# Optimization experiments

Measured on AMD Instinct MI355X. Metric: run time of the kernel, lower is better.

## Reference

```python
import jax, jax.numpy as jnp
import numpy as np

B, IN, H = 4096, 1024, 1024


def setup_inputs() -> dict:
    key = jax.random.key(0)
    ks = jax.random.split(key, 12)
    s = float(np.sqrt(6.0 / (IN + H)))  # xavier-uniform-like scale
    u = lambda k, shp: jax.random.uniform(k, shp, jnp.float32, -s, s)
    return {
        "x": jax.random.normal(ks[0], (B, IN), jnp.float32),
        "h_prev": jax.random.normal(ks[1], (B, H), jnp.float32),
        "c_prev": jax.random.normal(ks[2], (B, H), jnp.float32),
        "n_prev": jnp.ones((B, H), jnp.float32),
        "m_prev": jnp.zeros((B, H), jnp.float32),
        "Wi_x": u(ks[3], (H, IN)), "bi": jnp.zeros((H,), jnp.float32), "Wi_h": u(ks[4], (H, H)),
        "Wf_x": u(ks[5], (H, IN)), "bf": jnp.full((H,), 2.0, jnp.float32), "Wf_h": u(ks[6], (H, H)),
        "Wz_x": u(ks[7], (H, IN)), "bz": jnp.zeros((H,), jnp.float32), "Wz_h": u(ks[8], (H, H)),
        "Wo_x": u(ks[9], (H, IN)), "bo": jnp.zeros((H,), jnp.float32), "Wo_h": u(ks[10], (H, H)),
    }


def reference(x, h_prev, c_prev, n_prev, m_prev,
              Wi_x, bi, Wi_h, Wf_x, bf, Wf_h,
              Wz_x, bz, Wz_h, Wo_x, bo, Wo_h):
    # 8 projections (x-side with bias, h-side without), torch Linear: y = x @ W.T + b
    i_tilde = x @ Wi_x.T + bi + h_prev @ Wi_h.T
    f_aff   = x @ Wf_x.T + bf + h_prev @ Wf_h.T
    z_aff   = x @ Wz_x.T + bz + h_prev @ Wz_h.T
    o_aff   = x @ Wo_x.T + bo + h_prev @ Wo_h.T

    # forget_as_exp=False path: sigmoid forget gate, log-domain stabilizer
    log_f = jnp.log(jnp.clip(jax.nn.sigmoid(f_aff), 1e-8, None))
    m_t = jnp.maximum(log_f + m_prev, i_tilde)
    i_prime = jnp.exp(i_tilde - m_t)
    f_prime = jnp.exp(log_f + m_prev - m_t)

    z = jnp.tanh(z_aff)
    c_t = f_prime * c_prev + i_prime * z
    n_t = f_prime * n_prev + i_prime
    h_t = jax.nn.sigmoid(o_aff) * (c_t / jnp.clip(n_t, 1e-6, None))
    return h_t, c_t, n_t, m_t
```

## Files before the change

### kernel.cpp

```cpp
#include <hip/hip_runtime.h>
#include <stdint.h>


#define B_DIM 4096
#define K_DIM 2048

typedef __bf16 bf16x8 __attribute__((ext_vector_type(8)));
typedef float f32x4 __attribute__((ext_vector_type(4)));
typedef unsigned short ushort8 __attribute__((ext_vector_type(8)));

__device__ __forceinline__ unsigned short f2bf(float f) {
  unsigned u = __float_as_uint(f);
  u += 0x7fffu + ((u >> 16) & 1u);
  return (unsigned short)(u >> 16);
}
__device__ __forceinline__ float bf2f(unsigned short u) {
  return __uint_as_float(((unsigned)u) << 16);
}

__device__ __forceinline__ ushort8 load8_as_bf16(const void* base, size_t off, bool isbf) {
  if (isbf) return *(const ushort8*)((const unsigned short*)base + off);
  const float* f = (const float*)base + off;
  float4 v0 = ((const float4*)f)[0];
  float4 v1 = ((const float4*)f)[1];
  ushort8 o;
  o[0] = f2bf(v0.x); o[1] = f2bf(v0.y); o[2] = f2bf(v0.z); o[3] = f2bf(v0.w);
  o[4] = f2bf(v1.x); o[5] = f2bf(v1.y); o[6] = f2bf(v1.z); o[7] = f2bf(v1.w);
  return o;
}

__global__ void pack_all(const void* __restrict__ xv, const void* __restrict__ hv,
                         const void* __restrict__ Wix, const void* __restrict__ Wih,
                         const void* __restrict__ Wfx, const void* __restrict__ Wfh,
                         const void* __restrict__ Wzx, const void* __restrict__ Wzh,
                         const void* __restrict__ Wox, const void* __restrict__ Woh,
                         unsigned short* __restrict__ Apk, unsigned short* __restrict__ Bpk) {
  const int blk = blockIdx.x;
  const int lane = threadIdx.x & 63;
  const bool isA = blk < 4096;
  const unsigned* disc = (const unsigned*)(isA ? xv : Wix);
  int v = 0;
  if (lane < 32) {
    unsigned e = (disc[lane] >> 7) & 0xFFu;
    v = (e > (isA ? 129u : 122u)) ? 1 : 0;
  }
  const bool isbf = (__ballot(v) == 0ull);

  const int k = threadIdx.x * 8;
  if (isA) {
    const int m = blk;
    const void* src = (k < 1024) ? xv : hv;
    size_t off = (size_t)m * 1024 + (k & 1023);
    *(ushort8*)(Apk + (size_t)m * 2048 + k) = load8_as_bf16(src, off, isbf);
  } else {
    const int br = blk - 4096;
    const int g = (br >> 4) & 3;
    const int wrow = ((br >> 6) << 4) | (br & 15);
    const void* W;
    if (k < 1024) W = (g == 0) ? Wix : (g == 1) ? Wfx : (g == 2) ? Wzx : Wox;
    else          W = (g == 0) ? Wih : (g == 1) ? Wfh : (g == 2) ? Wzh : Woh;
    size_t off = (size_t)wrow * 1024 + (k & 1023);
    *(ushort8*)(Bpk + (size_t)br * 2048 + k) = load8_as_bf16(W, off, isbf);
  }
}


__device__ __forceinline__ void gload16(const unsigned short* g, unsigned short* l) {
  __builtin_amdgcn_global_load_lds(
      (__attribute__((address_space(1))) void*)g,
      (__attribute__((address_space(3))) void*)l, 16, 0, 0);
}

#define SCHED0 __builtin_amdgcn_sched_barrier(0)
#define BAR    __builtin_amdgcn_s_barrier()
#define VM4    asm volatile("s_waitcnt vmcnt(4)" ::: "memory")
#define VM0    asm volatile("s_waitcnt vmcnt(0)" ::: "memory")
#define NOWAIT ((void)0)
#define NOSTAGE ((void)0)
#define LGKM0  { asm volatile("s_waitcnt lgkmcnt(0)" ::: "memory"); SCHED0; }

#define STAGE_HALF(buf, ab, hf, kt) {                                          \
    _Pragma("unroll")                                                          \
    for (int r_ = 0; r_ < 2; ++r_) {                                           \
      const unsigned short* g_ = (ab ? sB : sA) +                              \
          (size_t)((r_ * 128 + (hf) * (ab ? 32 : 64)) * 2048 + (kt) * 64);     \
      gload16(g_, &lds[buf][ab][(hf) * 128 + r_ * 64 + w * 8][0]);             \
    } }

#define RD_A(buf, mh)                                                          \
  _Pragma("unroll")                                                            \
  for (int mi = 0; mi < 4; ++mi) {                                             \
    fA[mi][0] = *(const bf16x8*)(&lds[buf][0][0][0] + ((mh)*128 + mi*16)*64 + aBase + csw0); \
    fA[mi][1] = *(const bf16x8*)(&lds[buf][0][0][0] + ((mh)*128 + mi*16)*64 + aBase + csw1); \
  }
#define RD_B(buf, nh, FB)                                                      \
  _Pragma("unroll")                                                            \
  for (int nf = 0; nf < 2; ++nf) {                                             \
    FB[nf][0] = *(const bf16x8*)(&lds[buf][1][0][0] + ((nh)*128 + nf*16)*64 + bBase + csw0); \
    FB[nf][1] = *(const bf16x8*)(&lds[buf][1][0][0] + ((nh)*128 + nf*16)*64 + bBase + csw1); \
  }

#define MFMA_Q(mh, nh, FB) {                                                   \
    __builtin_amdgcn_s_setprio(1);                                             \
    _Pragma("unroll")                                                          \
    for (int mi = 0; mi < 4; ++mi)                                             \
      _Pragma("unroll")                                                        \
      for (int nf = 0; nf < 2; ++nf)                                           \
        _Pragma("unroll")                                                      \
        for (int ks = 0; ks < 2; ++ks)                                         \
          acc[(mh)*4 + mi][(nh)*2 + nf] = __builtin_amdgcn_mfma_f32_16x16x32_bf16( \
              fA[mi][ks], FB[nf][ks], acc[(mh)*4 + mi][(nh)*2 + nf], 0, 0, 0); \
    __builtin_amdgcn_s_setprio(0);                                             \
  }

#define PH(READS, STAGE, MF, WAIT) {                                           \
    READS; STAGE; SCHED0; BAR; LGKM0; MF; WAIT; SCHED0; BAR; SCHED0; }

__global__ __launch_bounds__(512, 2) void gemm_fused(
    const unsigned short* __restrict__ Apk,
    const unsigned short* __restrict__ Bpk,
    const void* __restrict__ bi, const void* __restrict__ bfg,
    const void* __restrict__ bz, const void* __restrict__ bo,
    const void* __restrict__ c_prev, const void* __restrict__ n_prev,
    const void* __restrict__ m_prev,
    float* __restrict__ out)
{
  __shared__ unsigned short lds[2][2][256][64];

  const int tid  = threadIdx.x;
  const int w    = tid >> 6;
  const int lane = tid & 63;
  const int wm   = w >> 2;
  const int wn   = w & 3;
  const int lcol = lane & 15;

  const int bid = blockIdx.x;
  const int swz = (bid & 7) * 32 + (bid >> 3);
  const int bm = swz >> 4;
  const int bn = swz & 15;

  const int l3 = lane >> 3;
  const int cg = (lane & 7) ^ l3;
  const unsigned short* sA = Apk + (size_t)(bm * 256 + w * 8 + l3) * 2048 + cg * 8;
  const unsigned short* sB = Bpk + (size_t)(bn * 256 + (w >> 2) * 64 + (w & 3) * 8 + l3) * 2048 + cg * 8;

  const int csw0 = (((lane >> 4)    ) ^ (lane & 7)) * 8;
  const int csw1 = ((4 + (lane >> 4)) ^ (lane & 7)) * 8;
  const int aBase = (wm * 64 + lcol) * 64;
  const int bBase = (wn * 32 + lcol) * 64;

  f32x4 acc[8][4] = {};
  bf16x8 fA[4][2], fB0[2][2], fB1[2][2];

  STAGE_HALF(0, 0, 0, 0); SCHED0;
  STAGE_HALF(0, 1, 0, 0); SCHED0;
  STAGE_HALF(0, 0, 1, 0); SCHED0;
  STAGE_HALF(0, 1, 1, 0); SCHED0;
  STAGE_HALF(1, 0, 0, 1); SCHED0;
  STAGE_HALF(1, 1, 0, 1); SCHED0;
  VM4; SCHED0; BAR; SCHED0;

  for (int t = 0; t < 30; t += 2) {
    PH({ RD_A(0, 0); RD_B(0, 0, fB0); }, STAGE_HALF(1, 1, 1, t + 1), MFMA_Q(0, 0, fB0), NOWAIT);
    PH({ RD_B(0, 1, fB1); },             STAGE_HALF(1, 0, 1, t + 1), MFMA_Q(0, 1, fB1), NOWAIT);
    PH({ RD_A(0, 1); },                  STAGE_HALF(0, 0, 0, t + 2), MFMA_Q(1, 1, fB1), NOWAIT);
    PH({ },                              STAGE_HALF(0, 1, 0, t + 2), MFMA_Q(1, 0, fB0), VM4);
    PH({ RD_A(1, 0); RD_B(1, 0, fB0); }, STAGE_HALF(0, 1, 1, t + 2), MFMA_Q(0, 0, fB0), NOWAIT);
    PH({ RD_B(1, 1, fB1); },             STAGE_HALF(0, 0, 1, t + 2), MFMA_Q(0, 1, fB1), NOWAIT);
    PH({ RD_A(1, 1); },                  STAGE_HALF(1, 0, 0, t + 3), MFMA_Q(1, 1, fB1), NOWAIT);
    PH({ },                              STAGE_HALF(1, 1, 0, t + 3), MFMA_Q(1, 0, fB0), VM4);
  }
  PH({ RD_A(0, 0); RD_B(0, 0, fB0); }, STAGE_HALF(1, 1, 1, 31), MFMA_Q(0, 0, fB0), NOWAIT);
  PH({ RD_B(0, 1, fB1); },             STAGE_HALF(1, 0, 1, 31), MFMA_Q(0, 1, fB1), NOWAIT);
  PH({ RD_A(0, 1); },                  NOSTAGE,                 MFMA_Q(1, 1, fB1), NOWAIT);
  PH({ },                              NOSTAGE,                 MFMA_Q(1, 0, fB0), VM0);
  PH({ RD_A(1, 0); RD_B(1, 0, fB0); }, NOSTAGE,                 MFMA_Q(0, 0, fB0), NOWAIT);
  PH({ RD_B(1, 1, fB1); },             NOSTAGE,                 MFMA_Q(0, 1, fB1), NOWAIT);
  PH({ RD_A(1, 1); },                  NOSTAGE,                 MFMA_Q(1, 1, fB1), NOWAIT);
  PH({ },                              NOSTAGE,                 MFMA_Q(1, 0, fB0), NOWAIT);

  const bool sbf = (((const unsigned*)n_prev)[0] == 0x3F803F80u);
  const bool bbf = (((const unsigned*)bfg)[0]    == 0x40004000u);
  const int n = (bn * 4 + wn) * 16 + lcol;
  const float bi_n = bbf ? bf2f(((const unsigned short*)bi)[n])  : ((const float*)bi)[n];
  const float bf_n = bbf ? bf2f(((const unsigned short*)bfg)[n]) : ((const float*)bfg)[n];
  const float bz_n = bbf ? bf2f(((const unsigned short*)bz)[n])  : ((const float*)bz)[n];
  const float bo_n = bbf ? bf2f(((const unsigned short*)bo)[n])  : ((const float*)bo)[n];
  const int row0 = bm * 256 + wm * 128 + (lane >> 4) * 4;

  float* out_h = out;
  float* out_c = out + 4194304;
  float* out_n = out + 2 * 4194304;
  float* out_m = out + 3 * 4194304;

#pragma unroll
  for (int mi = 0; mi < 8; ++mi) {
#pragma unroll
    for (int r = 0; r < 4; ++r) {
      const int row = row0 + mi * 16 + r;
      const size_t idx = (size_t)row * 1024 + n;
      float it = acc[mi][0][r] + bi_n;
      float fa = acc[mi][1][r] + bf_n;
      float za = acc[mi][2][r] + bz_n;
      float oa = acc[mi][3][r] + bo_n;
      float cp  = sbf ? bf2f(((const unsigned short*)c_prev)[idx]) : ((const float*)c_prev)[idx];
      float npv = sbf ? bf2f(((const unsigned short*)n_prev)[idx]) : ((const float*)n_prev)[idx];
      float mp  = sbf ? bf2f(((const unsigned short*)m_prev)[idx]) : ((const float*)m_prev)[idx];

      float sf = 1.f / (1.f + __expf(-fa));
      sf = fmaxf(sf, 1e-8f);
      float lf = __logf(sf);
      float mt = fmaxf(lf + mp, it);
      float ip = __expf(it - mt);
      float fp = __expf(lf + mp - mt);
      float zc = fminf(fmaxf(za, -15.f), 15.f);
      float e2 = __expf(2.f * zc);
      float z  = (e2 - 1.f) / (e2 + 1.f);
      float ct = fp * cp + ip * z;
      float nt = fp * npv + ip;
      float so = 1.f / (1.f + __expf(-oa));
      float ht = so * (ct / fmaxf(nt, 1e-6f));

      out_h[idx] = ht;
      out_c[idx] = ct;
      out_n[idx] = nt;
      out_m[idx] = mt;
    }
  }
}

extern "C" void kernel_launch(void* const* d_in, const int* in_sizes, int n_in,
                              void* d_out, int out_size, void* d_ws, size_t ws_size,
                              hipStream_t stream) {
  const void* x      = d_in[0];
  const void* h_prev = d_in[1];
  const void* c_prev = d_in[2];
  const void* n_prev = d_in[3];
  const void* m_prev = d_in[4];
  const void* Wi_x = d_in[5];
  const void* bi   = d_in[6];
  const void* Wi_h = d_in[7];
  const void* Wf_x = d_in[8];
  const void* bf   = d_in[9];
  const void* Wf_h = d_in[10];
  const void* Wz_x = d_in[11];
  const void* bz   = d_in[12];
  const void* Wz_h = d_in[13];
  const void* Wo_x = d_in[14];
  const void* bo   = d_in[15];
  const void* Wo_h = d_in[16];

  unsigned short* Apk = (unsigned short*)d_ws;
  unsigned short* Bpk = Apk + (size_t)B_DIM * K_DIM;

  pack_all<<<8192, 256, 0, stream>>>(x, h_prev, Wi_x, Wi_h, Wf_x, Wf_h,
                                     Wz_x, Wz_h, Wo_x, Wo_h, Apk, Bpk);
  gemm_fused<<<256, 512, 0, stream>>>(Apk, Bpk, bi, bf, bz, bo,
                                      c_prev, n_prev, m_prev,
                                      (float*)d_out);
}
```

Measured before the change: 253.3 us.

## Restructure GEMM main loop into four phases with partial lgkmcnt waits

Reorganizes the double-buffered MFMA main loop so each 64-wide K step reads all A-half-0 and both B fragments up front, then waits with partial lgkmcnt counts so the first MFMAs start before every LDS read completes. The second-half A reads are interleaved with the MFMAs of phase 2. The staging order of global-to-LDS loads is also reshuffled, with one more half staged in the prologue and the vmcnt threshold raised to 6. The aim is to hide LDS read latency behind matrix work; the risk is a race in buffer reuse or in the wait-count accounting if the stage order and the barriers do not line up.

```diff
diff --git a/kernel.cpp b/kernel.cpp
--- a/kernel.cpp
+++ b/kernel.cpp
@@ -73,11 +73,11 @@
 
 #define SCHED0 __builtin_amdgcn_sched_barrier(0)
 #define BAR    __builtin_amdgcn_s_barrier()
-#define VM4    asm volatile("s_waitcnt vmcnt(4)" ::: "memory")
+#define VM6    asm volatile("s_waitcnt vmcnt(6)" ::: "memory")
 #define VM0    asm volatile("s_waitcnt vmcnt(0)" ::: "memory")
+#define LGKM(N) asm volatile("s_waitcnt lgkmcnt(" #N ")" ::: "memory")
 #define NOWAIT ((void)0)
 #define NOSTAGE ((void)0)
-#define LGKM0  { asm volatile("s_waitcnt lgkmcnt(0)" ::: "memory"); SCHED0; }
 
 #define STAGE_HALF(buf, ab, hf, kt) {                                          \
     _Pragma("unroll")                                                          \
@@ -87,34 +87,75 @@
       gload16(g_, &lds[buf][ab][(hf) * 128 + r_ * 64 + w * 8][0]);             \
     } }
 
-#define RD_A(buf, mh)                                                          \
-  _Pragma("unroll")                                                            \
-  for (int mi = 0; mi < 4; ++mi) {                                             \
-    fA[mi][0] = *(const bf16x8*)(&lds[buf][0][0][0] + ((mh)*128 + mi*16)*64 + aBase + csw0); \
-    fA[mi][1] = *(const bf16x8*)(&lds[buf][0][0][0] + ((mh)*128 + mi*16)*64 + aBase + csw1); \
-  }
-#define RD_B(buf, nh, FB)                                                      \
-  _Pragma("unroll")                                                            \
-  for (int nf = 0; nf < 2; ++nf) {                                             \
-    FB[nf][0] = *(const bf16x8*)(&lds[buf][1][0][0] + ((nh)*128 + nf*16)*64 + bBase + csw0); \
-    FB[nf][1] = *(const bf16x8*)(&lds[buf][1][0][0] + ((nh)*128 + nf*16)*64 + bBase + csw1); \
-  }
-
-#define MFMA_Q(mh, nh, FB) {                                                   \
+#define LDSA(buf, mh, mi, CS) \
+  (*(const bf16x8*)(&lds[buf][0][0][0] + ((mh)*128 + (mi)*16)*64 + aBase + CS))
+#define LDSB(buf, nh, nf, CS) \
+  (*(const bf16x8*)(&lds[buf][1][0][0] + ((nh)*128 + (nf)*16)*64 + bBase + CS))
+
+#define RD16(buf) {                                                            \
+    fA[0][0]=LDSA(buf,0,0,csw0); fA[1][0]=LDSA(buf,0,1,csw0);                  \
+    fA[2][0]=LDSA(buf,0,2,csw0); fA[3][0]=LDSA(buf,0,3,csw0);                  \
+    fB0[0][0]=LDSB(buf,0,0,csw0); fB0[1][0]=LDSB(buf,0,1,csw0);                \
+    SCHED0;                                                                    \
+    fA[0][1]=LDSA(buf,0,0,csw1); fA[1][1]=LDSA(buf,0,1,csw1);                  \
+    fA[2][1]=LDSA(buf,0,2,csw1); fA[3][1]=LDSA(buf,0,3,csw1);                  \
+    fB0[0][1]=LDSB(buf,0,0,csw1); fB0[1][1]=LDSB(buf,0,1,csw1);                \
+    SCHED0;                                                                    \
+    fB1[0][0]=LDSB(buf,1,0,csw0); fB1[1][0]=LDSB(buf,1,1,csw0);                \
+    fB1[0][1]=LDSB(buf,1,0,csw1); fB1[1][1]=LDSB(buf,1,1,csw1);                \
+  }
+
+#define MFMA_H(FB, MH, NH, KS) {                                               \
     __builtin_amdgcn_s_setprio(1);                                             \
-    _Pragma("unroll")                                                          \
-    for (int mi = 0; mi < 4; ++mi)                                             \
-      _Pragma("unroll")                                                        \
-      for (int nf = 0; nf < 2; ++nf)                                           \
-        _Pragma("unroll")                                                      \
-        for (int ks = 0; ks < 2; ++ks)                                         \
-          acc[(mh)*4 + mi][(nh)*2 + nf] = __builtin_amdgcn_mfma_f32_16x16x32_bf16( \
-              fA[mi][ks], FB[nf][ks], acc[(mh)*4 + mi][(nh)*2 + nf], 0, 0, 0); \
-    __builtin_amdgcn_s_setprio(0);                                             \
-  }
-
-#define PH(READS, STAGE, MF, WAIT) {                                           \
-    READS; STAGE; SCHED0; BAR; LGKM0; MF; WAIT; SCHED0; BAR; SCHED0; }
+    _Pragma("unroll") for (int mi = 0; mi < 4; ++mi)                           \
+      _Pragma("unroll") for (int nf = 0; nf < 2; ++nf)                         \
+        acc[(MH)*4+mi][(NH)*2+nf] = __builtin_amdgcn_mfma_f32_16x16x32_bf16(   \
+            fA[mi][KS], FB[nf][KS], acc[(MH)*4+mi][(NH)*2+nf], 0, 0, 0);       \
+    __builtin_amdgcn_s_setprio(0); }
+
+#define MFMA_Q2(FB, MH, NH) {                                                  \
+    __builtin_amdgcn_s_setprio(1);                                             \
+    _Pragma("unroll") for (int mi = 0; mi < 4; ++mi)                           \
+      _Pragma("unroll") for (int nf = 0; nf < 2; ++nf)                         \
+        _Pragma("unroll") for (int ks = 0; ks < 2; ++ks)                       \
+          acc[(MH)*4+mi][(NH)*2+nf] = __builtin_amdgcn_mfma_f32_16x16x32_bf16( \
+              fA[mi][ks], FB[nf][ks], acc[(MH)*4+mi][(NH)*2+nf], 0, 0, 0);     \
+    __builtin_amdgcn_s_setprio(0); }
+
+#define PHASE1(buf, STG) {                                                     \
+    RD16(buf); SCHED0; STG; SCHED0; BAR;                                       \
+    LGKM(10); SCHED0;                                                          \
+    MFMA_H(fB0, 0, 0, 0); SCHED0;                                              \
+    LGKM(4); SCHED0;                                                           \
+    MFMA_H(fB0, 0, 0, 1); SCHED0;                                              \
+    BAR; SCHED0; }
+
+#define PHASE2(buf, STG) {                                                     \
+    STG; SCHED0; BAR;                                                          \
+    LGKM(0); SCHED0;                                                           \
+    __builtin_amdgcn_s_setprio(1);                                             \
+    _Pragma("unroll") for (int mi = 0; mi < 4; ++mi) {                         \
+      _Pragma("unroll") for (int nf = 0; nf < 2; ++nf)                         \
+        _Pragma("unroll") for (int ks = 0; ks < 2; ++ks)                       \
+          acc[mi][2+nf] = __builtin_amdgcn_mfma_f32_16x16x32_bf16(             \
+              fA[mi][ks], fB1[nf][ks], acc[mi][2+nf], 0, 0, 0);                \
+      fA[mi][0] = LDSA(buf, 1, mi, csw0);                                      \
+      fA[mi][1] = LDSA(buf, 1, mi, csw1);                                      \
+    }                                                                          \
+    __builtin_amdgcn_s_setprio(0); SCHED0;                                     \
+    BAR; SCHED0; }
+
+#define PHASE3(STG) {                                                          \
+    STG; SCHED0; BAR;                                                          \
+    LGKM(0); SCHED0;                                                           \
+    MFMA_Q2(fB1, 1, 1); SCHED0;                                                \
+    BAR; SCHED0; }
+
+#define PHASE4(STG, VMW) {                                                     \
+    STG; SCHED0; BAR;                                                          \
+    LGKM(0); SCHED0;                                                           \
+    MFMA_Q2(fB0, 1, 0); VMW; SCHED0;                                           \
+    BAR; SCHED0; }
 
 __global__ __launch_bounds__(512, 2) void gemm_fused(
     const unsigned short* __restrict__ Apk,
@@ -154,30 +195,31 @@
 
   STAGE_HALF(0, 0, 0, 0); SCHED0;
   STAGE_HALF(0, 1, 0, 0); SCHED0;
+  STAGE_HALF(0, 1, 1, 0); SCHED0;
   STAGE_HALF(0, 0, 1, 0); SCHED0;
-  STAGE_HALF(0, 1, 1, 0); SCHED0;
   STAGE_HALF(1, 0, 0, 1); SCHED0;
   STAGE_HALF(1, 1, 0, 1); SCHED0;
-  VM4; SCHED0; BAR; SCHED0;
+  STAGE_HALF(1, 1, 1, 1); SCHED0;
+  VM6; SCHED0; BAR; SCHED0;
 
   for (int t = 0; t < 30; t += 2) {
-    PH({ RD_A(0, 0); RD_B(0, 0, fB0); }, STAGE_HALF(1, 1, 1, t + 1), MFMA_Q(0, 0, fB0), NOWAIT);
-    PH({ RD_B(0, 1, fB1); },             STAGE_HALF(1, 0, 1, t + 1), MFMA_Q(0, 1, fB1), NOWAIT);
-    PH({ RD_A(0, 1); },                  STAGE_HALF(0, 0, 0, t + 2), MFMA_Q(1, 1, fB1), NOWAIT);
-    PH({ },                              STAGE_HALF(0, 1, 0, t + 2), MFMA_Q(1, 0, fB0), VM4);
-    PH({ RD_A(1, 0); RD_B(1, 0, fB0); }, STAGE_HALF(0, 1, 1, t + 2), MFMA_Q(0, 0, fB0), NOWAIT);
-    PH({ RD_B(1, 1, fB1); },             STAGE_HALF(0, 0, 1, t + 2), MFMA_Q(0, 1, fB1), NOWAIT);
-    PH({ RD_A(1, 1); },                  STAGE_HALF(1, 0, 0, t + 3), MFMA_Q(1, 1, fB1), NOWAIT);
-    PH({ },                              STAGE_HALF(1, 1, 0, t + 3), MFMA_Q(1, 0, fB0), VM4);
-  }
-  PH({ RD_A(0, 0); RD_B(0, 0, fB0); }, STAGE_HALF(1, 1, 1, 31), MFMA_Q(0, 0, fB0), NOWAIT);
-  PH({ RD_B(0, 1, fB1); },             STAGE_HALF(1, 0, 1, 31), MFMA_Q(0, 1, fB1), NOWAIT);
-  PH({ RD_A(0, 1); },                  NOSTAGE,                 MFMA_Q(1, 1, fB1), NOWAIT);
-  PH({ },                              NOSTAGE,                 MFMA_Q(1, 0, fB0), VM0);
-  PH({ RD_A(1, 0); RD_B(1, 0, fB0); }, NOSTAGE,                 MFMA_Q(0, 0, fB0), NOWAIT);
-  PH({ RD_B(1, 1, fB1); },             NOSTAGE,                 MFMA_Q(0, 1, fB1), NOWAIT);
-  PH({ RD_A(1, 1); },                  NOSTAGE,                 MFMA_Q(1, 1, fB1), NOWAIT);
-  PH({ },                              NOSTAGE,                 MFMA_Q(1, 0, fB0), NOWAIT);
+    PHASE1(0, STAGE_HALF(1, 0, 1, t + 1));
+    PHASE2(0, STAGE_HALF(0, 0, 0, t + 2));
+    PHASE3(   STAGE_HALF(0, 1, 0, t + 2));
+    PHASE4(   STAGE_HALF(0, 1, 1, t + 2), VM6);
+    PHASE1(1, STAGE_HALF(0, 0, 1, t + 2));
+    PHASE2(1, STAGE_HALF(1, 0, 0, t + 3));
+    PHASE3(   STAGE_HALF(1, 1, 0, t + 3));
+    PHASE4(   STAGE_HALF(1, 1, 1, t + 3), VM6);
+  }
+  PHASE1(0, STAGE_HALF(1, 0, 1, 31));
+  PHASE2(0, NOSTAGE);
+  PHASE3(   NOSTAGE);
+  PHASE4(   NOSTAGE, VM0);
+  PHASE1(1, NOSTAGE);
+  PHASE2(1, NOSTAGE);
+  PHASE3(   NOSTAGE);
+  PHASE4(   NOSTAGE, NOWAIT);
 
   const bool sbf = (((const unsigned*)n_prev)[0] == 0x3F803F80u);
   const bool bbf = (((const unsigned*)bfg)[0]    == 0x40004000u);
```

New measurement: 256.2 us. No clear change (+1.2%).
